# Kernel optimization log

Hardware: AMD Instinct MI355X
Metric: run time of the kernel (lower is better)

Reference implementation:

```python
import jax, jax.numpy as jnp
import numpy as np

N = 100000   # input nodes
M = 100000   # output nodes (size = (N, M))
NNZ = 3_200_000  # edges, avg_degree 32
B = 32       # batch
D = 32       # Kaiming channel dim


def setup_inputs() -> dict:
    key = jax.random.key(0)
    k1, k2, k3 = jax.random.split(key, 3)
    # COO indices: row 0 = src (in [0, N)), row 1 = dst (in [0, M))
    indices = jax.random.randint(k1, (2, NNZ), 0, N, dtype=jnp.int32)
    # Kaiming init: randn * sqrt(2/d), as in the torch module when d is given
    values = jax.random.normal(k2, (NNZ,), dtype=jnp.float32) * np.float32((2.0 / D) ** 0.5)
    bias = jnp.zeros((M, 1), dtype=jnp.float32)
    x = jax.random.normal(k3, (B, N, 1), dtype=jnp.float32)
    return {"x": x, "indices": indices, "values": values, "bias": bias}


def reference(x, indices, values, bias):
    # Equivalent of: for each b, sparse.mm(W.T, x[b]) + bias, W in COO (N, M)
    # y[b, m] = sum_{e: dst[e]==m} values[e] * x[b, src[e]] + bias[m]
    src = indices[0]
    dst = indices[1]
    contrib = x[:, src, 0] * values[None, :]           # (B, NNZ) gather-multiply
    y = jax.ops.segment_sum(contrib.T, dst, num_segments=M)  # (M, B) scatter-add
    return (y.T + bias[:, 0][None, :])[..., None]       # (B, M, 1)
```

## Files before the change

### kernel.cpp

```cpp
#include <hip/hip_runtime.h>
#include <hip/hip_fp16.h>
#include <stdint.h>

#define NB 32
#define BIN_SHIFT 5
#define BIN_ROWS 32
#define NBINS_MAX 4096
#define CSHIFT 8
#define NC_MAX 512
#define FPC 8
#define NWAVE 16
#define FCHUNK 8192
#define FTHREADS 1024
#define EPT (FCHUNK / FTHREADS)
#define CAP_C 9216
#define EPT2 (CAP_C / FTHREADS)
#define SRC_BITS 18
#define SRC_MASK ((1u << SRC_BITS) - 1)
#define CAP 1408
#define MAXK 6


__global__ void transpose_x_kernel(const float* __restrict__ x,
                                   __half* __restrict__ xt, int N) {
    __shared__ float tile[32][33];
    int n0 = blockIdx.x * 32;
    for (int i = threadIdx.y; i < 32; i += 8) {
        int n = n0 + threadIdx.x;
        tile[i][threadIdx.x] = (n < N) ? x[(size_t)i * N + n] : 0.f;
    }
    __syncthreads();
    for (int i = threadIdx.y; i < 32; i += 8) {
        int n = n0 + i;
        if (n < N) xt[(size_t)n * NB + threadIdx.x] =
            __float2half(tile[threadIdx.x][i]);
    }
}

__global__ void fill_coarse(const int* __restrict__ src,
                            const int* __restrict__ dst,
                            const float* __restrict__ vals,
                            int* __restrict__ cCursor,
                            uint2* __restrict__ cCsr,
                            int* __restrict__ ovCount,
                            int* __restrict__ ovList,
                            int nnz, int ncoarse) {
    __shared__ int lhist[NC_MAX];
    __shared__ int lbase[NC_MAX];
    int t = threadIdx.x;
    int e0 = blockIdx.x * FCHUNK;
    int dcache[EPT];
    for (int i = t; i < NC_MAX; i += FTHREADS) lhist[i] = 0;
    __syncthreads();
#pragma unroll
    for (int q = 0; q < EPT; ++q) {
        int e = e0 + q * FTHREADS + t;
        int d = (e < nnz) ? dst[e] : -1;
        dcache[q] = d;
        if (d >= 0) atomicAdd(&lhist[d >> CSHIFT], 1);
    }
    __syncthreads();
    for (int i = t; i < ncoarse; i += FTHREADS) {
        int c = lhist[i];
        lbase[i] = c ? atomicAdd(&cCursor[i], c) : 0;
        lhist[i] = 0;
    }
    __syncthreads();
#pragma unroll
    for (int q = 0; q < EPT; ++q) {
        int e = e0 + q * FTHREADS + t;
        int d = dcache[q];
        if (d >= 0) {
            int c = d >> CSHIFT;
            int r = lbase[c] + atomicAdd(&lhist[c], 1);
            if (r < CAP_C) {
                uint32_t meta = ((uint32_t)(d & 255) << SRC_BITS) |
                                (uint32_t)src[e];
                cCsr[(size_t)c * CAP_C + r] =
                    make_uint2(meta, __float_as_uint(vals[e]));
            } else {
                int op = atomicAdd(ovCount, 1);
                ovList[op] = e;
            }
        }
    }
}

__global__ __launch_bounds__(1024) void fill_fine2(
        const int* __restrict__ cCursor,
        const uint2* __restrict__ cCsr,
        uint2* __restrict__ fineCsr,
        int* __restrict__ fineBase,
        int* __restrict__ fineCnt) {
    __shared__ int whist[NWAVE][FPC];
    __shared__ int fbase[FPC];
    __shared__ int ftot;
    int c = blockIdx.x;
    int n = min(cCursor[c], CAP_C);
    int t = threadIdx.x;
    int w = t >> 6;
    uint2 ec[EPT2];
    if (t < NWAVE * FPC) (&whist[0][0])[t] = 0;
    __syncthreads();
    const uint2* reg = cCsr + (size_t)c * CAP_C;
#pragma unroll
    for (int q = 0; q < EPT2; ++q) {
        int j = q * FTHREADS + t;
        if (j < n) {
            uint2 e = reg[j];
            ec[q] = e;
            atomicAdd(&whist[w][(e.x >> 23) & 7], 1);
        }
    }
    __syncthreads();
    if (t == 0) {
        int run = 0;
        for (int f = 0; f < FPC; ++f) {
            fbase[f] = run;
            for (int w2 = 0; w2 < NWAVE; ++w2) {
                int cn = whist[w2][f];
                whist[w2][f] = run;
                run += cn;
            }
        }
        ftot = run;
    }
    __syncthreads();
    if (t < FPC) {
        int gbin = c * FPC + t;
        fineBase[gbin] = c * CAP_C + fbase[t];
        int endv = (t == FPC - 1) ? ftot : fbase[t + 1];
        fineCnt[gbin] = endv - fbase[t];
    }
#pragma unroll
    for (int q = 0; q < EPT2; ++q) {
        int j = q * FTHREADS + t;
        if (j < n) {
            uint2 e = ec[q];
            int p = atomicAdd(&whist[w][(e.x >> 23) & 7], 1);
            fineCsr[(size_t)c * CAP_C + p] = e;
        }
    }
}

__global__ __launch_bounds__(256) void sort_gather(
        const int* __restrict__ fineBase,
        const int* __restrict__ fineCnt,
        const uint2* __restrict__ csr,
        const __half* __restrict__ xt,
        const float* __restrict__ bias,
        float* __restrict__ out, int M) {
    __shared__ uint2 sorted[CAP];
    __shared__ int rowCnt[BIN_ROWS];
    __shared__ int rowOff[BIN_ROWS];
    int t = threadIdx.x;
    int bin = blockIdx.x;
    int start = fineBase[bin];
    int cnt   = fineCnt[bin];
    int g = t >> 5;
    int b = t & 31;

    if (cnt <= CAP) {
        uint2 reg[MAXK];
#pragma unroll
        for (int k = 0; k < MAXK; ++k) {
            int j = t + k * 256;
            if (j < cnt) reg[k] = csr[start + j];
        }
        if (t < BIN_ROWS) rowCnt[t] = 0;
        __syncthreads();
#pragma unroll
        for (int k = 0; k < MAXK; ++k) {
            int j = t + k * 256;
            if (j < cnt)
                atomicAdd(&rowCnt[(reg[k].x >> SRC_BITS) & 31], 1);
        }
        __syncthreads();
        if (t == 0) {
            int run = 0;
#pragma unroll
            for (int r = 0; r < BIN_ROWS; ++r) {
                rowOff[r] = run;
                run += rowCnt[r];
            }
        }
        __syncthreads();
#pragma unroll
        for (int k = 0; k < MAXK; ++k) {
            int j = t + k * 256;
            if (j < cnt) {
                int p = atomicAdd(&rowOff[(reg[k].x >> SRC_BITS) & 31], 1);
                sorted[p] = reg[k];
            }
        }
        __syncthreads();
        for (int r = g; r < BIN_ROWS; r += 8) {
            int m = bin * BIN_ROWS + r;
            if (m >= M) break;
            int jend = rowOff[r];
            int jj   = jend - rowCnt[r];
            float acc0 = 0.f, acc1 = 0.f;
            for (; jj + 8 <= jend; jj += 8) {
                uint2 e0 = sorted[jj + 0];
                uint2 e1 = sorted[jj + 1];
                uint2 e2 = sorted[jj + 2];
                uint2 e3 = sorted[jj + 3];
                uint2 e4 = sorted[jj + 4];
                uint2 e5 = sorted[jj + 5];
                uint2 e6 = sorted[jj + 6];
                uint2 e7 = sorted[jj + 7];
                float x0 = __half2float(xt[(size_t)(e0.x & SRC_MASK) * NB + b]);
                float x1 = __half2float(xt[(size_t)(e1.x & SRC_MASK) * NB + b]);
                float x2 = __half2float(xt[(size_t)(e2.x & SRC_MASK) * NB + b]);
                float x3 = __half2float(xt[(size_t)(e3.x & SRC_MASK) * NB + b]);
                float x4 = __half2float(xt[(size_t)(e4.x & SRC_MASK) * NB + b]);
                float x5 = __half2float(xt[(size_t)(e5.x & SRC_MASK) * NB + b]);
                float x6 = __half2float(xt[(size_t)(e6.x & SRC_MASK) * NB + b]);
                float x7 = __half2float(xt[(size_t)(e7.x & SRC_MASK) * NB + b]);
                acc0 = fmaf(__uint_as_float(e0.y), x0, acc0);
                acc1 = fmaf(__uint_as_float(e1.y), x1, acc1);
                acc0 = fmaf(__uint_as_float(e2.y), x2, acc0);
                acc1 = fmaf(__uint_as_float(e3.y), x3, acc1);
                acc0 = fmaf(__uint_as_float(e4.y), x4, acc0);
                acc1 = fmaf(__uint_as_float(e5.y), x5, acc1);
                acc0 = fmaf(__uint_as_float(e6.y), x6, acc0);
                acc1 = fmaf(__uint_as_float(e7.y), x7, acc1);
            }
            for (; jj < jend; ++jj) {
                uint2 e = sorted[jj];
                acc0 = fmaf(__uint_as_float(e.y),
                            __half2float(xt[(size_t)(e.x & SRC_MASK) * NB + b]),
                            acc0);
            }
            out[(size_t)b * M + m] = acc0 + acc1 + bias[m];
        }
    } else {
        float* tile = (float*)sorted;
        for (int i = t; i < BIN_ROWS * NB; i += 256) tile[i] = 0.f;
        __syncthreads();
        for (int j = start + g; j < start + cnt; j += 8) {
            uint2 e = csr[j];
            float xv = __half2float(xt[(size_t)(e.x & SRC_MASK) * NB + b]);
            atomicAdd(&tile[((e.x >> SRC_BITS) & 31) * NB + b],
                      __uint_as_float(e.y) * xv);
        }
        __syncthreads();
        for (int i = t; i < BIN_ROWS * NB; i += 256) {
            int m = bin * BIN_ROWS + (i >> 5);
            if (m < M) out[(size_t)(i & 31) * M + m] = tile[i] + bias[m];
        }
    }
}

__global__ void fixup_kernel(const int* __restrict__ ovCount,
                             const int* __restrict__ ovList,
                             const int* __restrict__ src,
                             const int* __restrict__ dst,
                             const float* __restrict__ vals,
                             const __half* __restrict__ xt,
                             float* __restrict__ out, int M) {
    long long total = (long long)(*ovCount) * 32;
    long long stride = (long long)gridDim.x * blockDim.x;
    for (long long i = (long long)blockIdx.x * blockDim.x + threadIdx.x;
         i < total; i += stride) {
        int k = (int)(i >> 5);
        int b = (int)(i & 31);
        int e = ovList[k];
        atomicAdd(&out[(size_t)b * M + dst[e]],
                  vals[e] * __half2float(xt[(size_t)src[e] * NB + b]));
    }
}

__global__ void finalize_kernel(const float* __restrict__ yt,
                                const float* __restrict__ bias,
                                float* __restrict__ out, int M) {
    __shared__ float tile[32][33];
    int m0 = blockIdx.x * 32;
    for (int i = threadIdx.y; i < 32; i += 8) {
        int m = m0 + i;
        tile[i][threadIdx.x] = (m < M) ? yt[(size_t)m * NB + threadIdx.x] : 0.f;
    }
    __syncthreads();
    for (int i = threadIdx.y; i < 32; i += 8) {
        int m = m0 + threadIdx.x;
        if (m < M) out[(size_t)i * M + m] = tile[threadIdx.x][i] + bias[m];
    }
}

__global__ void scatter_kernel(const int* __restrict__ src,
                               const int* __restrict__ dst,
                               const float* __restrict__ vals,
                               const __half* __restrict__ xt,
                               float* __restrict__ yt, int nnz) {
    long long tid = (long long)blockIdx.x * blockDim.x + threadIdx.x;
    int e = (int)(tid >> 5);
    if (e >= nnz) return;
    int b = (int)(tid & 31);
    atomicAdd(&yt[(size_t)dst[e] * NB + b],
              vals[e] * __half2float(xt[(size_t)src[e] * NB + b]));
}

extern "C" void kernel_launch(void* const* d_in, const int* in_sizes, int n_in,
                              void* d_out, int out_size, void* d_ws, size_t ws_size,
                              hipStream_t stream) {
    const float* x       = (const float*)d_in[0];
    const int*   indices = (const int*)  d_in[1];
    const float* vals    = (const float*)d_in[2];
    const float* bias    = (const float*)d_in[3];

    float* out = (float*)d_out;

    int nnz = in_sizes[1] / 2;
    int N   = in_sizes[0] / NB;
    int M   = in_sizes[3];

    const int* src = indices;
    const int* dst = indices + nnz;

    int nbins   = (M + BIN_ROWS - 1) >> BIN_SHIFT;
    int ncoarse = (M + (1 << CSHIFT) - 1) >> CSHIFT;

    __half* xt       = (__half*)d_ws;
    int*    cCursor  = (int*)(xt + (size_t)N * NB);
    int*    ovCount  = cCursor + NC_MAX;
    int*    fineBase = ovCount + 4;
    int*    fineCnt  = fineBase + NBINS_MAX;
    int*    ovList   = fineCnt + NBINS_MAX;
    uint2*  cCsr     = (uint2*)(((uintptr_t)(ovList + nnz) + 15) &
                                ~(uintptr_t)15);
    uint2*  fineCsr  = cCsr + (size_t)ncoarse * CAP_C;

    size_t need = (size_t)((char*)(fineCsr + (size_t)ncoarse * CAP_C) -
                           (char*)d_ws);

    float* yt = (float*)(xt + (size_t)N * NB);
    size_t need_fb = (size_t)((char*)(yt + (size_t)M * NB) - (char*)d_ws);

    transpose_x_kernel<<<(N + 31) / 32, dim3(32, 8), 0, stream>>>(x, xt, N);

    if (ws_size >= need && nbins <= NBINS_MAX && ncoarse <= NC_MAX) {
        hipMemsetAsync(cCursor, 0, (NC_MAX + 4) * sizeof(int), stream);
        int fgrid = (nnz + FCHUNK - 1) / FCHUNK;
        fill_coarse<<<fgrid, FTHREADS, 0, stream>>>(src, dst, vals, cCursor,
                                                    cCsr, ovCount, ovList,
                                                    nnz, ncoarse);
        fill_fine2<<<ncoarse, FTHREADS, 0, stream>>>(cCursor, cCsr, fineCsr,
                                                     fineBase, fineCnt);
        sort_gather<<<nbins, 256, 0, stream>>>(fineBase, fineCnt, fineCsr,
                                               xt, bias, out, M);
        fixup_kernel<<<32, 256, 0, stream>>>(ovCount, ovList, src, dst, vals,
                                             xt, out, M);
    } else if (ws_size >= need_fb) {
        hipMemsetAsync(yt, 0, (size_t)M * NB * sizeof(float), stream);
        long long pairs = (long long)nnz * NB;
        int grid = (int)((pairs + 255) / 256);
        scatter_kernel<<<grid, 256, 0, stream>>>(src, dst, vals, xt, yt, nnz);
        finalize_kernel<<<(M + 31) / 32, dim3(32, 8), 0, stream>>>(yt, bias,
                                                                   out, M);
    }
}
```

Baseline: 215.2 us.

## Sort edges to full per-row CSR in fill_fine and gather per row directly

The second binning pass now sorts edges by exact destination row (256 rows per coarse bin) and writes per-row base and count arrays. This lets the gather kernel read each row's edges straight from global memory with no per-block shared-memory re-sort. fill_coarse now stages its chunk in shared memory, ordered by coarse bin through a prefix scan, so its global writes are contiguous runs. The cursor memset is folded into the transpose kernel. The cost is larger shared-memory histograms and scans in the fill kernels and a bigger shared footprint in fill_coarse, which may reduce occupancy.

```diff
diff --git a/kernel.cpp b/kernel.cpp
--- a/kernel.cpp
+++ b/kernel.cpp
@@ -3,12 +3,9 @@
 #include <stdint.h>
 
 #define NB 32
-#define BIN_SHIFT 5
-#define BIN_ROWS 32
-#define NBINS_MAX 4096
 #define CSHIFT 8
+#define CROWS 256
 #define NC_MAX 512
-#define FPC 8
 #define NWAVE 16
 #define FCHUNK 8192
 #define FTHREADS 1024
@@ -17,13 +14,17 @@
 #define EPT2 (CAP_C / FTHREADS)
 #define SRC_BITS 18
 #define SRC_MASK ((1u << SRC_BITS) - 1)
-#define CAP 1408
-#define MAXK 6
+#define GT 512
 
 
 __global__ void transpose_x_kernel(const float* __restrict__ x,
-                                   __half* __restrict__ xt, int N) {
+                                   __half* __restrict__ xt,
+                                   int* __restrict__ zeroRegion, int N) {
     __shared__ float tile[32][33];
+    if (blockIdx.x == 0) {
+        int i = threadIdx.y * 32 + threadIdx.x;
+        for (; i < NC_MAX + 4; i += 256) zeroRegion[i] = 0;
+    }
     int n0 = blockIdx.x * 32;
     for (int i = threadIdx.y; i < 32; i += 8) {
         int n = n0 + threadIdx.x;
@@ -37,52 +38,82 @@
     }
 }
 
-__global__ void fill_coarse(const int* __restrict__ src,
-                            const int* __restrict__ dst,
-                            const float* __restrict__ vals,
-                            int* __restrict__ cCursor,
-                            uint2* __restrict__ cCsr,
-                            int* __restrict__ ovCount,
-                            int* __restrict__ ovList,
-                            int nnz, int ncoarse) {
+__global__ __launch_bounds__(1024) void fill_coarse(
+        const int* __restrict__ src,
+        const int* __restrict__ dst,
+        const float* __restrict__ vals,
+        int* __restrict__ cCursor,
+        uint2* __restrict__ csr,
+        int* __restrict__ ovCount,
+        int* __restrict__ ovList,
+        int nnz) {
+    __shared__ uint2 stage[FCHUNK];
+    __shared__ unsigned short binOf[FCHUNK];
     __shared__ int lhist[NC_MAX];
     __shared__ int lbase[NC_MAX];
+    __shared__ int delta[NC_MAX];
+    __shared__ int sscan[NC_MAX];
     int t = threadIdx.x;
     int e0 = blockIdx.x * FCHUNK;
-    int dcache[EPT];
+    int chunk = min(FCHUNK, nnz - e0);
+    int dcache[EPT], scache[EPT];
+    float vcache[EPT];
     for (int i = t; i < NC_MAX; i += FTHREADS) lhist[i] = 0;
     __syncthreads();
 #pragma unroll
     for (int q = 0; q < EPT; ++q) {
         int e = e0 + q * FTHREADS + t;
-        int d = (e < nnz) ? dst[e] : -1;
-        dcache[q] = d;
-        if (d >= 0) atomicAdd(&lhist[d >> CSHIFT], 1);
-    }
-    __syncthreads();
-    for (int i = t; i < ncoarse; i += FTHREADS) {
-        int c = lhist[i];
-        lbase[i] = c ? atomicAdd(&cCursor[i], c) : 0;
-        lhist[i] = 0;
+        if (e < nnz) {
+            int d = dst[e];
+            dcache[q] = d;
+            scache[q] = src[e];
+            vcache[q] = vals[e];
+            atomicAdd(&lhist[d >> CSHIFT], 1);
+        } else dcache[q] = -1;
+    }
+    __syncthreads();
+    int v = (t < NC_MAX) ? lhist[t] : 0;
+    if (t < NC_MAX) sscan[t] = v;
+    __syncthreads();
+    for (int off = 1; off < NC_MAX; off <<= 1) {
+        int add = (t < NC_MAX && t >= off) ? sscan[t - off] : 0;
+        __syncthreads();
+        if (t < NC_MAX) sscan[t] += add;
+        __syncthreads();
+    }
+    if (t < NC_MAX) {
+        int excl = sscan[t] - v;
+        lbase[t] = excl;
+        int grel = v ? atomicAdd(&cCursor[t], v) : 0;
+        delta[t] = grel - excl;
+        lhist[t] = 0;
     }
     __syncthreads();
 #pragma unroll
     for (int q = 0; q < EPT; ++q) {
-        int e = e0 + q * FTHREADS + t;
         int d = dcache[q];
         if (d >= 0) {
-            int c = d >> CSHIFT;
-            int r = lbase[c] + atomicAdd(&lhist[c], 1);
-            if (r < CAP_C) {
-                uint32_t meta = ((uint32_t)(d & 255) << SRC_BITS) |
-                                (uint32_t)src[e];
-                cCsr[(size_t)c * CAP_C + r] =
-                    make_uint2(meta, __float_as_uint(vals[e]));
+            int bin = d >> CSHIFT;
+            int r = atomicAdd(&lhist[bin], 1);
+            int pos = lbase[bin] + r;
+            if (delta[bin] + pos < CAP_C) {
+                stage[pos] = make_uint2(
+                    ((uint32_t)(d & (CROWS - 1)) << SRC_BITS) |
+                        (uint32_t)scache[q],
+                    __float_as_uint(vcache[q]));
+                binOf[pos] = (unsigned short)bin;
             } else {
+                binOf[pos] = 0xFFFF;
                 int op = atomicAdd(ovCount, 1);
-                ovList[op] = e;
+                ovList[op] = e0 + q * FTHREADS + t;
             }
         }
+    }
+    __syncthreads();
+    for (int idx = t; idx < chunk; idx += FTHREADS) {
+        unsigned short bo = binOf[idx];
+        if (bo != 0xFFFF)
+            csr[(size_t)bo * CAP_C + delta[bo] + idx] = stage[idx];
     }
 }
 
@@ -90,17 +121,17 @@
         const int* __restrict__ cCursor,
         const uint2* __restrict__ cCsr,
         uint2* __restrict__ fineCsr,
-        int* __restrict__ fineBase,
-        int* __restrict__ fineCnt) {
-    __shared__ int whist[NWAVE][FPC];
-    __shared__ int fbase[FPC];
-    __shared__ int ftot;
+        int* __restrict__ rowBase,
+        int* __restrict__ rowCnt, int M) {
+    __shared__ int whist[NWAVE][CROWS];
+    __shared__ int fbase[CROWS];
+    __shared__ int sscan[CROWS];
     int c = blockIdx.x;
     int n = min(cCursor[c], CAP_C);
     int t = threadIdx.x;
     int w = t >> 6;
     uint2 ec[EPT2];
-    if (t < NWAVE * FPC) (&whist[0][0])[t] = 0;
+    for (int i = t; i < NWAVE * CROWS; i += FTHREADS) (&whist[0][0])[i] = 0;
     __syncthreads();
     const uint2* reg = cCsr + (size_t)c * CAP_C;
 #pragma unroll
@@ -109,147 +140,98 @@
         if (j < n) {
             uint2 e = reg[j];
             ec[q] = e;
-            atomicAdd(&whist[w][(e.x >> 23) & 7], 1);
-        }
-    }
-    __syncthreads();
-    if (t == 0) {
-        int run = 0;
-        for (int f = 0; f < FPC; ++f) {
-            fbase[f] = run;
-            for (int w2 = 0; w2 < NWAVE; ++w2) {
-                int cn = whist[w2][f];
-                whist[w2][f] = run;
-                run += cn;
-            }
-        }
-        ftot = run;
-    }
-    __syncthreads();
-    if (t < FPC) {
-        int gbin = c * FPC + t;
-        fineBase[gbin] = c * CAP_C + fbase[t];
-        int endv = (t == FPC - 1) ? ftot : fbase[t + 1];
-        fineCnt[gbin] = endv - fbase[t];
-    }
+            atomicAdd(&whist[w][(e.x >> SRC_BITS) & (CROWS - 1)], 1);
+        }
+    }
+    __syncthreads();
+    int tot = 0;
+    if (t < CROWS) {
+#pragma unroll
+        for (int w2 = 0; w2 < NWAVE; ++w2) tot += whist[w2][t];
+        sscan[t] = tot;
+    }
+    __syncthreads();
+    for (int off = 1; off < CROWS; off <<= 1) {
+        int add = (t < CROWS && t >= off) ? sscan[t - off] : 0;
+        __syncthreads();
+        if (t < CROWS) sscan[t] += add;
+        __syncthreads();
+    }
+    if (t < CROWS) {
+        int excl = sscan[t] - tot;
+        fbase[t] = excl;
+        int m = c * CROWS + t;
+        if (m < M) {
+            rowBase[m] = c * CAP_C + excl;
+            rowCnt[m]  = tot;
+        }
+        int run = excl;
+#pragma unroll
+        for (int w2 = 0; w2 < NWAVE; ++w2) {
+            int cn = whist[w2][t];
+            whist[w2][t] = run;
+            run += cn;
+        }
+    }
+    __syncthreads();
 #pragma unroll
     for (int q = 0; q < EPT2; ++q) {
         int j = q * FTHREADS + t;
         if (j < n) {
             uint2 e = ec[q];
-            int p = atomicAdd(&whist[w][(e.x >> 23) & 7], 1);
+            int p = atomicAdd(&whist[w][(e.x >> SRC_BITS) & (CROWS - 1)], 1);
             fineCsr[(size_t)c * CAP_C + p] = e;
         }
     }
 }
 
-__global__ __launch_bounds__(256) void sort_gather(
-        const int* __restrict__ fineBase,
-        const int* __restrict__ fineCnt,
+__global__ __launch_bounds__(GT) void row_gather(
+        const int* __restrict__ rowBase,
+        const int* __restrict__ rowCnt,
         const uint2* __restrict__ csr,
         const __half* __restrict__ xt,
         const float* __restrict__ bias,
         float* __restrict__ out, int M) {
-    __shared__ uint2 sorted[CAP];
-    __shared__ int rowCnt[BIN_ROWS];
-    __shared__ int rowOff[BIN_ROWS];
-    int t = threadIdx.x;
-    int bin = blockIdx.x;
-    int start = fineBase[bin];
-    int cnt   = fineCnt[bin];
-    int g = t >> 5;
-    int b = t & 31;
-
-    if (cnt <= CAP) {
-        uint2 reg[MAXK];
-#pragma unroll
-        for (int k = 0; k < MAXK; ++k) {
-            int j = t + k * 256;
-            if (j < cnt) reg[k] = csr[start + j];
-        }
-        if (t < BIN_ROWS) rowCnt[t] = 0;
-        __syncthreads();
-#pragma unroll
-        for (int k = 0; k < MAXK; ++k) {
-            int j = t + k * 256;
-            if (j < cnt)
-                atomicAdd(&rowCnt[(reg[k].x >> SRC_BITS) & 31], 1);
-        }
-        __syncthreads();
-        if (t == 0) {
-            int run = 0;
-#pragma unroll
-            for (int r = 0; r < BIN_ROWS; ++r) {
-                rowOff[r] = run;
-                run += rowCnt[r];
-            }
-        }
-        __syncthreads();
-#pragma unroll
-        for (int k = 0; k < MAXK; ++k) {
-            int j = t + k * 256;
-            if (j < cnt) {
-                int p = atomicAdd(&rowOff[(reg[k].x >> SRC_BITS) & 31], 1);
-                sorted[p] = reg[k];
-            }
-        }
-        __syncthreads();
-        for (int r = g; r < BIN_ROWS; r += 8) {
-            int m = bin * BIN_ROWS + r;
-            if (m >= M) break;
-            int jend = rowOff[r];
-            int jj   = jend - rowCnt[r];
-            float acc0 = 0.f, acc1 = 0.f;
-            for (; jj + 8 <= jend; jj += 8) {
-                uint2 e0 = sorted[jj + 0];
-                uint2 e1 = sorted[jj + 1];
-                uint2 e2 = sorted[jj + 2];
-                uint2 e3 = sorted[jj + 3];
-                uint2 e4 = sorted[jj + 4];
-                uint2 e5 = sorted[jj + 5];
-                uint2 e6 = sorted[jj + 6];
-                uint2 e7 = sorted[jj + 7];
-                float x0 = __half2float(xt[(size_t)(e0.x & SRC_MASK) * NB + b]);
-                float x1 = __half2float(xt[(size_t)(e1.x & SRC_MASK) * NB + b]);
-                float x2 = __half2float(xt[(size_t)(e2.x & SRC_MASK) * NB + b]);
-                float x3 = __half2float(xt[(size_t)(e3.x & SRC_MASK) * NB + b]);
-                float x4 = __half2float(xt[(size_t)(e4.x & SRC_MASK) * NB + b]);
-                float x5 = __half2float(xt[(size_t)(e5.x & SRC_MASK) * NB + b]);
-                float x6 = __half2float(xt[(size_t)(e6.x & SRC_MASK) * NB + b]);
-                float x7 = __half2float(xt[(size_t)(e7.x & SRC_MASK) * NB + b]);
-                acc0 = fmaf(__uint_as_float(e0.y), x0, acc0);
-                acc1 = fmaf(__uint_as_float(e1.y), x1, acc1);
-                acc0 = fmaf(__uint_as_float(e2.y), x2, acc0);
-                acc1 = fmaf(__uint_as_float(e3.y), x3, acc1);
-                acc0 = fmaf(__uint_as_float(e4.y), x4, acc0);
-                acc1 = fmaf(__uint_as_float(e5.y), x5, acc1);
-                acc0 = fmaf(__uint_as_float(e6.y), x6, acc0);
-                acc1 = fmaf(__uint_as_float(e7.y), x7, acc1);
-            }
-            for (; jj < jend; ++jj) {
-                uint2 e = sorted[jj];
-                acc0 = fmaf(__uint_as_float(e.y),
-                            __half2float(xt[(size_t)(e.x & SRC_MASK) * NB + b]),
-                            acc0);
-            }
-            out[(size_t)b * M + m] = acc0 + acc1 + bias[m];
-        }
-    } else {
-        float* tile = (float*)sorted;
-        for (int i = t; i < BIN_ROWS * NB; i += 256) tile[i] = 0.f;
-        __syncthreads();
-        for (int j = start + g; j < start + cnt; j += 8) {
-            uint2 e = csr[j];
-            float xv = __half2float(xt[(size_t)(e.x & SRC_MASK) * NB + b]);
-            atomicAdd(&tile[((e.x >> SRC_BITS) & 31) * NB + b],
-                      __uint_as_float(e.y) * xv);
-        }
-        __syncthreads();
-        for (int i = t; i < BIN_ROWS * NB; i += 256) {
-            int m = bin * BIN_ROWS + (i >> 5);
-            if (m < M) out[(size_t)(i & 31) * M + m] = tile[i] + bias[m];
-        }
-    }
+    int g = threadIdx.x >> 5;
+    int b = threadIdx.x & 31;
+    int m = blockIdx.x * (GT / 32) + g;
+    if (m >= M) return;
+    int j   = rowBase[m];
+    int end = j + rowCnt[m];
+    float acc0 = 0.f, acc1 = 0.f;
+    for (; j + 8 <= end; j += 8) {
+        uint2 e0 = csr[j + 0];
+        uint2 e1 = csr[j + 1];
+        uint2 e2 = csr[j + 2];
+        uint2 e3 = csr[j + 3];
+        uint2 e4 = csr[j + 4];
+        uint2 e5 = csr[j + 5];
+        uint2 e6 = csr[j + 6];
+        uint2 e7 = csr[j + 7];
+        float x0 = __half2float(xt[(size_t)(e0.x & SRC_MASK) * NB + b]);
+        float x1 = __half2float(xt[(size_t)(e1.x & SRC_MASK) * NB + b]);
+        float x2 = __half2float(xt[(size_t)(e2.x & SRC_MASK) * NB + b]);
+        float x3 = __half2float(xt[(size_t)(e3.x & SRC_MASK) * NB + b]);
+        float x4 = __half2float(xt[(size_t)(e4.x & SRC_MASK) * NB + b]);
+        float x5 = __half2float(xt[(size_t)(e5.x & SRC_MASK) * NB + b]);
+        float x6 = __half2float(xt[(size_t)(e6.x & SRC_MASK) * NB + b]);
+        float x7 = __half2float(xt[(size_t)(e7.x & SRC_MASK) * NB + b]);
+        acc0 = fmaf(__uint_as_float(e0.y), x0, acc0);
+        acc1 = fmaf(__uint_as_float(e1.y), x1, acc1);
+        acc0 = fmaf(__uint_as_float(e2.y), x2, acc0);
+        acc1 = fmaf(__uint_as_float(e3.y), x3, acc1);
+        acc0 = fmaf(__uint_as_float(e4.y), x4, acc0);
+        acc1 = fmaf(__uint_as_float(e5.y), x5, acc1);
+        acc0 = fmaf(__uint_as_float(e6.y), x6, acc0);
+        acc1 = fmaf(__uint_as_float(e7.y), x7, acc1);
+    }
+    for (; j < end; ++j) {
+        uint2 e = csr[j];
+        acc0 = fmaf(__uint_as_float(e.y),
+                    __half2float(xt[(size_t)(e.x & SRC_MASK) * NB + b]),
+                    acc0);
+    }
+    out[(size_t)b * M + m] = acc0 + acc1 + bias[m];
 }
 
 __global__ void fixup_kernel(const int* __restrict__ ovCount,
@@ -317,18 +299,17 @@
     const int* src = indices;
     const int* dst = indices + nnz;
 
-    int nbins   = (M + BIN_ROWS - 1) >> BIN_SHIFT;
-    int ncoarse = (M + (1 << CSHIFT) - 1) >> CSHIFT;
-
-    __half* xt       = (__half*)d_ws;
-    int*    cCursor  = (int*)(xt + (size_t)N * NB);
-    int*    ovCount  = cCursor + NC_MAX;
-    int*    fineBase = ovCount + 4;
-    int*    fineCnt  = fineBase + NBINS_MAX;
-    int*    ovList   = fineCnt + NBINS_MAX;
-    uint2*  cCsr     = (uint2*)(((uintptr_t)(ovList + nnz) + 15) &
-                                ~(uintptr_t)15);
-    uint2*  fineCsr  = cCsr + (size_t)ncoarse * CAP_C;
+    int ncoarse = (M + CROWS - 1) >> CSHIFT;
+
+    __half* xt      = (__half*)d_ws;
+    int*    cCursor = (int*)(xt + (size_t)N * NB);
+    int*    ovCount = cCursor + NC_MAX;
+    int*    rowBase = ovCount + 4;
+    int*    rowCnt  = rowBase + M;
+    int*    ovList  = rowCnt + M;
+    uint2*  cCsr    = (uint2*)(((uintptr_t)(ovList + nnz) + 15) &
+                               ~(uintptr_t)15);
+    uint2*  fineCsr = cCsr + (size_t)ncoarse * CAP_C;
 
     size_t need = (size_t)((char*)(fineCsr + (size_t)ncoarse * CAP_C) -
                            (char*)d_ws);
@@ -336,21 +317,22 @@
     float* yt = (float*)(xt + (size_t)N * NB);
     size_t need_fb = (size_t)((char*)(yt + (size_t)M * NB) - (char*)d_ws);
 
-    transpose_x_kernel<<<(N + 31) / 32, dim3(32, 8), 0, stream>>>(x, xt, N);
-
-    if (ws_size >= need && nbins <= NBINS_MAX && ncoarse <= NC_MAX) {
-        hipMemsetAsync(cCursor, 0, (NC_MAX + 4) * sizeof(int), stream);
+    if (ws_size >= need && ncoarse <= NC_MAX) {
+        transpose_x_kernel<<<(N + 31) / 32, dim3(32, 8), 0, stream>>>(
+            x, xt, cCursor, N);
         int fgrid = (nnz + FCHUNK - 1) / FCHUNK;
         fill_coarse<<<fgrid, FTHREADS, 0, stream>>>(src, dst, vals, cCursor,
                                                     cCsr, ovCount, ovList,
-                                                    nnz, ncoarse);
+                                                    nnz);
         fill_fine2<<<ncoarse, FTHREADS, 0, stream>>>(cCursor, cCsr, fineCsr,
-                                                     fineBase, fineCnt);
-        sort_gather<<<nbins, 256, 0, stream>>>(fineBase, fineCnt, fineCsr,
-                                               xt, bias, out, M);
+                                                     rowBase, rowCnt, M);
+        row_gather<<<(M + GT / 32 - 1) / (GT / 32), GT, 0, stream>>>(
+            rowBase, rowCnt, fineCsr, xt, bias, out, M);
         fixup_kernel<<<32, 256, 0, stream>>>(ovCount, ovList, src, dst, vals,
                                              xt, out, M);
     } else if (ws_size >= need_fb) {
+        transpose_x_kernel<<<(N + 31) / 32, dim3(32, 8), 0, stream>>>(
+            x, xt, cCursor, N);
         hipMemsetAsync(yt, 0, (size_t)M * NB * sizeof(float), stream);
         long long pairs = (long long)nnz * NB;
         int grid = (int)((pairs + 255) / 256);
```

Result: faster. 205.1 us (-4.7%).
